# Optimization experiments

Hardware: AMD Instinct MI355X
Metric: run time of the kernel (lower is better)

## Reference

```python
import jax, jax.numpy as jnp
import numpy as np

B, T, C = 4, 2048, 768
H = 12  # n_head; head_dim = C // H = 64


def setup_inputs() -> dict:
    key = jax.random.key(0)
    k1, k2, k3, k4, k5 = jax.random.split(key, 5)
    scale = 0.02
    return {
        "x": jax.random.normal(k1, (B, T, C), dtype=jnp.float32),
        "w_attn": jax.random.normal(k2, (C, 3 * C), dtype=jnp.float32) * scale,
        "b_attn": jax.random.normal(k3, (3 * C,), dtype=jnp.float32) * scale,
        "w_proj": jax.random.normal(k4, (C, C), dtype=jnp.float32) * scale,
        "b_proj": jax.random.normal(k5, (C,), dtype=jnp.float32) * scale,
    }


def reference(x, w_attn, b_attn, w_proj, b_proj):
    Bx, Tx, Cx = x.shape
    hd = Cx // H  # head dim
    qkv = x @ w_attn + b_attn                       # [B, T, 3C]
    q, k, v = jnp.split(qkv, 3, axis=2)
    # [B, T, H, hd] -> [B, H, T, hd]
    q = q.reshape(Bx, Tx, H, hd).transpose(0, 2, 1, 3)
    k = k.reshape(Bx, Tx, H, hd).transpose(0, 2, 1, 3)
    v = v.reshape(Bx, Tx, H, hd).transpose(0, 2, 1, 3)
    att = jnp.einsum('bhqd,bhkd->bhqk', q, k) / jnp.sqrt(jnp.float32(hd))
    causal = jnp.tril(jnp.ones((Tx, Tx), dtype=bool))
    att = jnp.where(causal[None, None, :, :], att, -jnp.inf)
    att = jax.nn.softmax(att, axis=-1)
    y = jnp.einsum('bhqk,bhkd->bhqd', att, v)       # [B, H, T, hd]
    y = y.transpose(0, 2, 1, 3).reshape(Bx, Tx, Cx)
    return y @ w_proj + b_proj
```

## Files before the change

kernel.cpp:

```cpp
#include <hip/hip_runtime.h>
#include <hip/hip_bf16.h>

using f32x4 = __attribute__((ext_vector_type(4))) float;
using s16x8 = __attribute__((ext_vector_type(8))) short;

#define MFMA16x16x32(a, b, c) __builtin_amdgcn_mfma_f32_16x16x32_bf16((a), (b), (c), 0, 0, 0)

#define AS_G(p) ((const __attribute__((address_space(1))) void*)(p))
#define AS_L(p) ((__attribute__((address_space(3))) void*)(p))

#define BARRIER_LGKM() do { \
    asm volatile("s_waitcnt lgkmcnt(0)" ::: "memory"); \
    __builtin_amdgcn_s_barrier(); \
} while (0)

static __device__ __forceinline__ unsigned short f2bf(float f) {
    unsigned int u = __float_as_uint(f);
    u = (u + 0x7fffu + ((u >> 16) & 1u)) >> 16;
    return (unsigned short)u;
}
static __device__ __forceinline__ unsigned int cvt_pk_bf2(float lo, float hi) {
    unsigned int r;
    asm("v_cvt_pk_bf16_f32 %0, %1, %2" : "=v"(r) : "v"(lo), "v"(hi));
    return r;
}
static __device__ __forceinline__ int swz128(int r, int c) { return (r * 128 + c) ^ ((r & 7) << 4); }

__global__ __launch_bounds__(256)
void prologue_kernel(const float* __restrict__ x, unsigned short* __restrict__ xb,
                     const float* __restrict__ w_attn, unsigned short* __restrict__ wTa,
                     const float* __restrict__ w_proj, unsigned short* __restrict__ wTp) {
    __shared__ float tile[32][33];
    const int bid = blockIdx.x, tid = threadIdx.x;
    if (bid < 2048) {
        const int n = 8192 * 768;
        int i = (bid * 256 + tid) * 4;
        const int stride = 2048 * 256 * 4;
        for (; i < n; i += stride) {
            float4 v = *(const float4*)(x + i);
            ushort4 o;
            o.x = f2bf(v.x); o.y = f2bf(v.y); o.z = f2bf(v.z); o.w = f2bf(v.w);
            *(ushort4*)(xb + i) = o;
        }
    } else {
        const float* w; unsigned short* wt; int K, N, bx, by;
        if (bid < 3776) {
            int id = bid - 2048; w = w_attn; wt = wTa; K = 768; N = 2304;
            bx = id % 72; by = id / 72;
        } else {
            int id = bid - 3776; w = w_proj; wt = wTp; K = 768; N = 768;
            bx = id % 24; by = id / 24;
        }
        const int tx = tid & 31, ty = tid >> 5;
        const int n0 = bx * 32, k0 = by * 32;
#pragma unroll
        for (int r = 0; r < 4; r++)
            tile[ty * 4 + r][tx] = w[(size_t)(k0 + ty * 4 + r) * N + n0 + tx];
        __syncthreads();
#pragma unroll
        for (int r = 0; r < 4; r++)
            wt[(size_t)(n0 + ty * 4 + r) * K + k0 + tx] = f2bf(tile[tx][ty * 4 + r]);
    }
}

template <bool OUT_BF16>
__global__ __launch_bounds__(256, 2)
void gemm_bt(const unsigned short* __restrict__ A, const unsigned short* __restrict__ Bt,
             const float* __restrict__ bias, void* __restrict__ Cout,
             unsigned short* __restrict__ Vt,
             int M, int N, int K, int ldc, int qcols, float qscale) {
    __shared__ char smem[65536];
    const int tid = threadIdx.x, wid = tid >> 6, lane = tid & 63;
    const int g = lane >> 4, lr = lane & 15;
    const int m0 = blockIdx.y * 128, n0 = blockIdx.x * 128;
    const int wm = wid >> 1, wn = wid & 1;

    f32x4 acc[4][4];
#pragma unroll
    for (int i = 0; i < 4; i++)
#pragma unroll
        for (int j = 0; j < 4; j++) acc[i][j] = f32x4{0.f, 0.f, 0.f, 0.f};

    const int rbase = lane >> 3;
    const int cSw = ((lane & 7) << 4) ^ (rbase << 4);

    auto STAGE = [&](int buf, int kt) {
        char* base = smem + buf * 32768;
#pragma unroll
        for (int ww = 0; ww < 4; ww++) {
            int w = wid * 4 + ww;
            int r = w * 8 + rbase;
            const unsigned short* srcA = A + (size_t)(m0 + r) * K + kt + (cSw >> 1);
            __builtin_amdgcn_global_load_lds(AS_G(srcA), AS_L(base + w * 1024), 16, 0, 0);
            const unsigned short* srcB = Bt + (size_t)(n0 + r) * K + kt + (cSw >> 1);
            __builtin_amdgcn_global_load_lds(AS_G(srcB), AS_L(base + 16384 + w * 1024), 16, 0, 0);
        }
    };

    const int nk = K >> 6;
    STAGE(0, 0);

    for (int t = 0; t < nk; t++) {
        if (t + 1 < nk) {
            STAGE((t + 1) & 1, (t + 1) << 6);
            asm volatile("s_waitcnt vmcnt(8)" ::: "memory");
        } else {
            asm volatile("s_waitcnt vmcnt(0)" ::: "memory");
        }
        __builtin_amdgcn_s_barrier();
        char* cbase = smem + (t & 1) * 32768;
#pragma unroll
        for (int ks = 0; ks < 2; ks++) {
            s16x8 af[4], bfr[4];
#pragma unroll
            for (int i = 0; i < 4; i++)
                af[i] = *(const s16x8*)(cbase + swz128(wm * 64 + i * 16 + lr, ks * 64 + g * 16));
#pragma unroll
            for (int j = 0; j < 4; j++)
                bfr[j] = *(const s16x8*)(cbase + 16384 + swz128(wn * 64 + j * 16 + lr, ks * 64 + g * 16));
#pragma unroll
            for (int i = 0; i < 4; i++)
#pragma unroll
                for (int j = 0; j < 4; j++)
                    acc[i][j] = MFMA16x16x32(af[i], bfr[j], acc[i][j]);
        }
        BARRIER_LGKM();
    }

#pragma unroll
    for (int j = 0; j < 4; j++) {
        int c = n0 + wn * 64 + j * 16 + lr;
        float bv = bias[c];
        float cscale = (c < qcols) ? qscale : 1.0f;
        if (Vt != nullptr && c >= 1536) {
            int h = (c - 1536) >> 6, d = (c - 1536) & 63;
#pragma unroll
            for (int i = 0; i < 4; i++) {
                int r0 = m0 + wm * 64 + i * 16 + g * 4;
                int bb = r0 >> 11, t0 = r0 & 2047;
                ushort4 o4;
                o4.x = f2bf(acc[i][j][0] + bv);
                o4.y = f2bf(acc[i][j][1] + bv);
                o4.z = f2bf(acc[i][j][2] + bv);
                o4.w = f2bf(acc[i][j][3] + bv);
                *(ushort4*)(Vt + ((((size_t)bb * 12 + h) * 64 + d) << 11) + t0) = o4;
            }
        } else {
#pragma unroll
            for (int i = 0; i < 4; i++) {
#pragma unroll
                for (int rg = 0; rg < 4; rg++) {
                    int r = m0 + wm * 64 + i * 16 + g * 4 + rg;
                    float val = (acc[i][j][rg] + bv) * cscale;
                    if constexpr (OUT_BF16)
                        ((unsigned short*)Cout)[(size_t)r * ldc + c] = f2bf(val);
                    else
                        ((float*)Cout)[(size_t)r * ldc + c] = val;
                }
            }
        }
    }
}

__global__ __launch_bounds__(256, 2)
void attn_kernel(const unsigned short* __restrict__ qk, const unsigned short* __restrict__ Vt,
                 unsigned short* __restrict__ y) {
    __shared__ char smem[49152];
    const int tid = threadIdx.x, wid = tid >> 6, lane = tid & 63;
    const int g = lane >> 4, lr = lane & 15;
    const int T = 2048;

    const int s = blockIdx.x;
    const int xcd = s & 7, i = s >> 3;
    const int grp = xcd * 6 + (i >> 4);
    const int qpi = i & 15;
    const int h = grp % 12, b = grp / 12;
    const int qtA = qpi, qtB = 31 - qpi;
    const int q0A = qtA * 64, q0B = qtB * 64;

    const int krow = tid >> 2;
    const int kcol = (tid & 3) * 32;

    s16x8 vone;
#pragma unroll
    for (int e = 0; e < 8; e++) vone[e] = (short)0x3F80;

    const unsigned short* qrowA = qk + (size_t)(b * T + q0A + wid * 16 + lr) * 1536 + h * 64;
    const unsigned short* qrowB = qk + (size_t)(b * T + q0B + wid * 16 + lr) * 1536 + h * 64;
    s16x8 aqA[2], aqB[2];
    aqA[0] = *(const s16x8*)(qrowA + g * 8);
    aqA[1] = *(const s16x8*)(qrowA + 32 + g * 8);
    aqB[0] = *(const s16x8*)(qrowB + g * 8);
    aqB[1] = *(const s16x8*)(qrowB + 32 + g * 8);

    f32x4 oA[4], oB[4], lsumA, lsumB;
#pragma unroll
    for (int r = 0; r < 4; r++) { oA[r] = f32x4{0.f, 0.f, 0.f, 0.f}; oB[r] = f32x4{0.f, 0.f, 0.f, 0.f}; }
    lsumA = f32x4{0.f, 0.f, 0.f, 0.f};
    lsumB = f32x4{0.f, 0.f, 0.f, 0.f};

    const unsigned short* pkBase = qk + (size_t)(b * T + krow) * 1536 + 768 + h * 64 + (kcol >> 1);
    const unsigned short* pvBase = Vt + ((((size_t)b * 12 + h) * 64 + krow) << 11) + (kcol >> 1);

    const int ntA = qtA + 1, ntB = qtB + 1;

    s16x8 k0 = *(const s16x8*)(pkBase);
    s16x8 k1 = *(const s16x8*)(pkBase + 8);
    s16x8 v0 = *(const s16x8*)(pvBase);
    s16x8 v1 = *(const s16x8*)(pvBase + 8);
    *(s16x8*)(smem + swz128(krow, kcol)) = k0;
    *(s16x8*)(smem + swz128(krow, kcol + 16)) = k1;
    *(s16x8*)(smem + 16384 + swz128(krow, kcol)) = v0;
    *(s16x8*)(smem + 16384 + swz128(krow, kcol + 16)) = v1;
    if (ntB > 1) {
        const unsigned short* pk = pkBase + (size_t)64 * 1536;
        k0 = *(const s16x8*)(pk);
        k1 = *(const s16x8*)(pk + 8);
        const unsigned short* pv = pvBase + 64;
        v0 = *(const s16x8*)(pv);
        v1 = *(const s16x8*)(pv + 8);
    }
    BARRIER_LGKM();

    char* const pbaseB = smem + 32768 + wid * 2048;
    char* const pbaseA = smem + 40960 + wid * 2048;
    const int q_rel = wid * 16 + lr;

    for (int t = 0; t < ntB; t++) {
        char* kbase = smem + (t & 1) * 8192;
        char* vbase = smem + 16384 + (t & 1) * 8192;
        const bool actA = (t < ntA);

        {
            f32x4 st[4];
            __builtin_amdgcn_s_setprio(1);
#pragma unroll
            for (int nf = 0; nf < 4; nf++) {
                f32x4 sf = f32x4{0.f, 0.f, 0.f, 0.f};
#pragma unroll
                for (int ks = 0; ks < 2; ks++) {
                    s16x8 ak = *(const s16x8*)(kbase + swz128(nf * 16 + lr, (ks * 32 + g * 8) * 2));
                    sf = MFMA16x16x32(ak, aqB[ks], sf);
                }
                st[nf] = sf;
            }
            __builtin_amdgcn_s_setprio(0);
            const bool diag = (t == ntB - 1);
#pragma unroll
            for (int nf = 0; nf < 4; nf++)
#pragma unroll
                for (int rg = 0; rg < 4; rg++) {
                    float p = __builtin_amdgcn_exp2f(st[nf][rg]);
                    if (diag && (nf * 16 + g * 4 + rg > q_rel)) p = 0.f;
                    st[nf][rg] = p;
                }
#pragma unroll
            for (int nf = 0; nf < 4; nf++) {
                uint2 dw;
                dw.x = cvt_pk_bf2(st[nf][0], st[nf][1]);
                dw.y = cvt_pk_bf2(st[nf][2], st[nf][3]);
                *(uint2*)(pbaseB + swz128(lr, nf * 32 + g * 8)) = dw;
            }
        }
        if (actA) {
            f32x4 st[4];
            __builtin_amdgcn_s_setprio(1);
#pragma unroll
            for (int nf = 0; nf < 4; nf++) {
                f32x4 sf = f32x4{0.f, 0.f, 0.f, 0.f};
#pragma unroll
                for (int ks = 0; ks < 2; ks++) {
                    s16x8 ak = *(const s16x8*)(kbase + swz128(nf * 16 + lr, (ks * 32 + g * 8) * 2));
                    sf = MFMA16x16x32(ak, aqA[ks], sf);
                }
                st[nf] = sf;
            }
            __builtin_amdgcn_s_setprio(0);
            const bool diag = (t == ntA - 1);
#pragma unroll
            for (int nf = 0; nf < 4; nf++)
#pragma unroll
                for (int rg = 0; rg < 4; rg++) {
                    float p = __builtin_amdgcn_exp2f(st[nf][rg]);
                    if (diag && (nf * 16 + g * 4 + rg > q_rel)) p = 0.f;
                    st[nf][rg] = p;
                }
#pragma unroll
            for (int nf = 0; nf < 4; nf++) {
                uint2 dw;
                dw.x = cvt_pk_bf2(st[nf][0], st[nf][1]);
                dw.y = cvt_pk_bf2(st[nf][2], st[nf][3]);
                *(uint2*)(pbaseA + swz128(lr, nf * 32 + g * 8)) = dw;
            }
        }

        {
            s16x8 pf[2];
#pragma unroll
            for (int ks = 0; ks < 2; ks++)
                pf[ks] = *(const s16x8*)(pbaseB + swz128(lr, ks * 64 + g * 16));
            __builtin_amdgcn_s_setprio(1);
#pragma unroll
            for (int nf = 0; nf < 4; nf++) {
#pragma unroll
                for (int ks = 0; ks < 2; ks++) {
                    s16x8 bv = *(const s16x8*)(vbase + swz128(nf * 16 + lr, ks * 64 + g * 16));
                    oB[nf] = MFMA16x16x32(pf[ks], bv, oB[nf]);
                }
            }
            lsumB = MFMA16x16x32(pf[0], vone, lsumB);
            lsumB = MFMA16x16x32(pf[1], vone, lsumB);
            __builtin_amdgcn_s_setprio(0);
        }
        if (actA) {
            s16x8 pf[2];
#pragma unroll
            for (int ks = 0; ks < 2; ks++)
                pf[ks] = *(const s16x8*)(pbaseA + swz128(lr, ks * 64 + g * 16));
            __builtin_amdgcn_s_setprio(1);
#pragma unroll
            for (int nf = 0; nf < 4; nf++) {
#pragma unroll
                for (int ks = 0; ks < 2; ks++) {
                    s16x8 bv = *(const s16x8*)(vbase + swz128(nf * 16 + lr, ks * 64 + g * 16));
                    oA[nf] = MFMA16x16x32(pf[ks], bv, oA[nf]);
                }
            }
            lsumA = MFMA16x16x32(pf[0], vone, lsumA);
            lsumA = MFMA16x16x32(pf[1], vone, lsumA);
            __builtin_amdgcn_s_setprio(0);
        }

        if (t + 1 < ntB) {
            char* kn = smem + ((t + 1) & 1) * 8192;
            char* vn = smem + 16384 + ((t + 1) & 1) * 8192;
            *(s16x8*)(kn + swz128(krow, kcol)) = k0;
            *(s16x8*)(kn + swz128(krow, kcol + 16)) = k1;
            *(s16x8*)(vn + swz128(krow, kcol)) = v0;
            *(s16x8*)(vn + swz128(krow, kcol + 16)) = v1;
            if (t + 2 < ntB) {
                const unsigned short* pk = pkBase + (size_t)(t + 2) * 64 * 1536;
                k0 = *(const s16x8*)(pk);
                k1 = *(const s16x8*)(pk + 8);
                const unsigned short* pv = pvBase + (t + 2) * 64;
                v0 = *(const s16x8*)(pv);
                v1 = *(const s16x8*)(pv + 8);
            }
        }
        BARRIER_LGKM();
    }

#pragma unroll
    for (int which = 0; which < 2; which++) {
        const f32x4 lsum = which ? lsumB : lsumA;
        const int q0 = which ? q0B : q0A;
        f32x4* o = which ? oB : oA;
        float linv_q[4];
#pragma unroll
        for (int rg = 0; rg < 4; rg++) linv_q[rg] = 1.0f / lsum[rg];
#pragma unroll
        for (int nf = 0; nf < 4; nf++) {
#pragma unroll
            for (int rg = 0; rg < 4; rg++) {
                int row = b * T + q0 + wid * 16 + g * 4 + rg;
                int col = h * 64 + nf * 16 + lr;
                y[(size_t)row * 768 + col] = f2bf(o[nf][rg] * linv_q[rg]);
            }
        }
    }
}

extern "C" void kernel_launch(void* const* d_in, const int* in_sizes, int n_in,
                              void* d_out, int out_size, void* d_ws, size_t ws_size,
                              hipStream_t stream) {
    const float* x      = (const float*)d_in[0];
    const float* w_attn = (const float*)d_in[1];
    const float* b_attn = (const float*)d_in[2];
    const float* w_proj = (const float*)d_in[3];
    const float* b_proj = (const float*)d_in[4];

    char* ws = (char*)d_ws;
    unsigned short* qk  = (unsigned short*)(ws);
    unsigned short* Vt  = (unsigned short*)(ws + 25165824);
    unsigned short* wTa = (unsigned short*)(ws + 37748736);
    unsigned short* wTp = (unsigned short*)(ws + 41287680);

    const bool big = ws_size >= (size_t)55050240;
    unsigned short* xb = (unsigned short*)d_out;
    unsigned short* yb = big ? (unsigned short*)(ws + 42467328)
                             : (unsigned short*)((char*)d_out + 12582912);
    float* projOut = big ? (float*)d_out : (float*)ws;

    prologue_kernel<<<4352, 256, 0, stream>>>(x, xb, w_attn, wTa, w_proj, wTp);

    gemm_bt<true><<<dim3(18, 64), 256, 0, stream>>>(xb, wTa, b_attn, (void*)qk, Vt,
                                                    8192, 2304, 768, 1536, 768, 0.1803368801111244f);
    attn_kernel<<<768, 256, 0, stream>>>(qk, Vt, yb);
    gemm_bt<false><<<dim3(6, 64), 256, 0, stream>>>(yb, wTp, b_proj, (void*)projOut, nullptr,
                                                    8192, 768, 768, 768, 0, 1.0f);
    if (!big)
        hipMemcpyAsync(d_out, projOut, 25165824, hipMemcpyDeviceToDevice, stream);
}
```

Baseline: 123.8 us.

## Remap GEMM blocks per XCD and interleave two query tiles' MFMAs in attention

The GEMM launch becomes a 1D grid. Each block's (m0, n0) is derived from blockIdx so that consecutive blocks landing on the same XCD share an M-row band, which is meant to improve L2 reuse of the A rows on the chiplet. In the attention loop, the QK^T and PV MFMAs for the two query tiles (A and B) are merged into single loops. Each K/V fragment read from LDS is then fed to both tiles, which halves those LDS reads and gives the scheduler independent MFMA chains to interleave. The cost is more live registers, since both score sets are held at once, plus a predicated actA branch inside the inner loops.

Measured after the change: 126.1 us. About the same (+1.8%).

```diff
diff --git a/kernel.cpp b/kernel.cpp
--- a/kernel.cpp
+++ b/kernel.cpp
@@ -72,7 +72,11 @@
     __shared__ char smem[65536];
     const int tid = threadIdx.x, wid = tid >> 6, lane = tid & 63;
     const int g = lane >> 4, lr = lane & 15;
-    const int m0 = blockIdx.y * 128, n0 = blockIdx.x * 128;
+    const int nx = N >> 7;
+    const int ypx = (M >> 7) >> 3;
+    const int xcd = blockIdx.x & 7, ii = blockIdx.x >> 3;
+    const int m0 = (xcd * ypx + ii / nx) * 128;
+    const int n0 = (ii % nx) * 128;
     const int wm = wid >> 1, wn = wid & 1;
 
     f32x4 acc[4][4];
@@ -231,105 +235,86 @@
         char* vbase = smem + 16384 + (t & 1) * 8192;
         const bool actA = (t < ntA);
 
+        f32x4 stB[4], stA[4];
+        __builtin_amdgcn_s_setprio(1);
+#pragma unroll
+        for (int nf = 0; nf < 4; nf++) {
+            f32x4 sB = f32x4{0.f, 0.f, 0.f, 0.f};
+            f32x4 sA = f32x4{0.f, 0.f, 0.f, 0.f};
+#pragma unroll
+            for (int ks = 0; ks < 2; ks++) {
+                s16x8 ak = *(const s16x8*)(kbase + swz128(nf * 16 + lr, (ks * 32 + g * 8) * 2));
+                sB = MFMA16x16x32(ak, aqB[ks], sB);
+                if (actA) sA = MFMA16x16x32(ak, aqA[ks], sA);
+            }
+            stB[nf] = sB;
+            stA[nf] = sA;
+        }
+        __builtin_amdgcn_s_setprio(0);
+
         {
-            f32x4 st[4];
-            __builtin_amdgcn_s_setprio(1);
-#pragma unroll
-            for (int nf = 0; nf < 4; nf++) {
-                f32x4 sf = f32x4{0.f, 0.f, 0.f, 0.f};
-#pragma unroll
-                for (int ks = 0; ks < 2; ks++) {
-                    s16x8 ak = *(const s16x8*)(kbase + swz128(nf * 16 + lr, (ks * 32 + g * 8) * 2));
-                    sf = MFMA16x16x32(ak, aqB[ks], sf);
-                }
-                st[nf] = sf;
-            }
-            __builtin_amdgcn_s_setprio(0);
             const bool diag = (t == ntB - 1);
 #pragma unroll
             for (int nf = 0; nf < 4; nf++)
 #pragma unroll
                 for (int rg = 0; rg < 4; rg++) {
-                    float p = __builtin_amdgcn_exp2f(st[nf][rg]);
+                    float p = __builtin_amdgcn_exp2f(stB[nf][rg]);
                     if (diag && (nf * 16 + g * 4 + rg > q_rel)) p = 0.f;
-                    st[nf][rg] = p;
+                    stB[nf][rg] = p;
                 }
 #pragma unroll
             for (int nf = 0; nf < 4; nf++) {
                 uint2 dw;
-                dw.x = cvt_pk_bf2(st[nf][0], st[nf][1]);
-                dw.y = cvt_pk_bf2(st[nf][2], st[nf][3]);
+                dw.x = cvt_pk_bf2(stB[nf][0], stB[nf][1]);
+                dw.y = cvt_pk_bf2(stB[nf][2], stB[nf][3]);
                 *(uint2*)(pbaseB + swz128(lr, nf * 32 + g * 8)) = dw;
             }
         }
         if (actA) {
-            f32x4 st[4];
-            __builtin_amdgcn_s_setprio(1);
-#pragma unroll
-            for (int nf = 0; nf < 4; nf++) {
-                f32x4 sf = f32x4{0.f, 0.f, 0.f, 0.f};
-#pragma unroll
-                for (int ks = 0; ks < 2; ks++) {
-                    s16x8 ak = *(const s16x8*)(kbase + swz128(nf * 16 + lr, (ks * 32 + g * 8) * 2));
-                    sf = MFMA16x16x32(ak, aqA[ks], sf);
-                }
-                st[nf] = sf;
-            }
-            __builtin_amdgcn_s_setprio(0);
             const bool diag = (t == ntA - 1);
 #pragma unroll
             for (int nf = 0; nf < 4; nf++)
 #pragma unroll
                 for (int rg = 0; rg < 4; rg++) {
-                    float p = __builtin_amdgcn_exp2f(st[nf][rg]);
+                    float p = __builtin_amdgcn_exp2f(stA[nf][rg]);
                     if (diag && (nf * 16 + g * 4 + rg > q_rel)) p = 0.f;
-                    st[nf][rg] = p;
+                    stA[nf][rg] = p;
                 }
 #pragma unroll
             for (int nf = 0; nf < 4; nf++) {
                 uint2 dw;
-                dw.x = cvt_pk_bf2(st[nf][0], st[nf][1]);
-                dw.y = cvt_pk_bf2(st[nf][2], st[nf][3]);
+                dw.x = cvt_pk_bf2(stA[nf][0], stA[nf][1]);
+                dw.y = cvt_pk_bf2(stA[nf][2], stA[nf][3]);
                 *(uint2*)(pbaseA + swz128(lr, nf * 32 + g * 8)) = dw;
             }
         }
 
-        {
-            s16x8 pf[2];
+        s16x8 pfB[2], pfA[2];
+#pragma unroll
+        for (int ks = 0; ks < 2; ks++)
+            pfB[ks] = *(const s16x8*)(pbaseB + swz128(lr, ks * 64 + g * 16));
+        if (actA) {
 #pragma unroll
             for (int ks = 0; ks < 2; ks++)
-                pf[ks] = *(const s16x8*)(pbaseB + swz128(lr, ks * 64 + g * 16));
-            __builtin_amdgcn_s_setprio(1);
-#pragma unroll
-            for (int nf = 0; nf < 4; nf++) {
-#pragma unroll
-                for (int ks = 0; ks < 2; ks++) {
-                    s16x8 bv = *(const s16x8*)(vbase + swz128(nf * 16 + lr, ks * 64 + g * 16));
-                    oB[nf] = MFMA16x16x32(pf[ks], bv, oB[nf]);
-                }
-            }
-            lsumB = MFMA16x16x32(pf[0], vone, lsumB);
-            lsumB = MFMA16x16x32(pf[1], vone, lsumB);
-            __builtin_amdgcn_s_setprio(0);
-        }
+                pfA[ks] = *(const s16x8*)(pbaseA + swz128(lr, ks * 64 + g * 16));
+        }
+        __builtin_amdgcn_s_setprio(1);
+#pragma unroll
+        for (int nf = 0; nf < 4; nf++) {
+#pragma unroll
+            for (int ks = 0; ks < 2; ks++) {
+                s16x8 bv = *(const s16x8*)(vbase + swz128(nf * 16 + lr, ks * 64 + g * 16));
+                oB[nf] = MFMA16x16x32(pfB[ks], bv, oB[nf]);
+                if (actA) oA[nf] = MFMA16x16x32(pfA[ks], bv, oA[nf]);
+            }
+        }
+        lsumB = MFMA16x16x32(pfB[0], vone, lsumB);
+        lsumB = MFMA16x16x32(pfB[1], vone, lsumB);
         if (actA) {
-            s16x8 pf[2];
-#pragma unroll
-            for (int ks = 0; ks < 2; ks++)
-                pf[ks] = *(const s16x8*)(pbaseA + swz128(lr, ks * 64 + g * 16));
-            __builtin_amdgcn_s_setprio(1);
-#pragma unroll
-            for (int nf = 0; nf < 4; nf++) {
-#pragma unroll
-                for (int ks = 0; ks < 2; ks++) {
-                    s16x8 bv = *(const s16x8*)(vbase + swz128(nf * 16 + lr, ks * 64 + g * 16));
-                    oA[nf] = MFMA16x16x32(pf[ks], bv, oA[nf]);
-                }
-            }
-            lsumA = MFMA16x16x32(pf[0], vone, lsumA);
-            lsumA = MFMA16x16x32(pf[1], vone, lsumA);
-            __builtin_amdgcn_s_setprio(0);
-        }
+            lsumA = MFMA16x16x32(pfA[0], vone, lsumA);
+            lsumA = MFMA16x16x32(pfA[1], vone, lsumA);
+        }
+        __builtin_amdgcn_s_setprio(0);
 
         if (t + 1 < ntB) {
             char* kn = smem + ((t + 1) & 1) * 8192;
@@ -393,11 +378,11 @@
 
     prologue_kernel<<<4352, 256, 0, stream>>>(x, xb, w_attn, wTa, w_proj, wTp);
 
-    gemm_bt<true><<<dim3(18, 64), 256, 0, stream>>>(xb, wTa, b_attn, (void*)qk, Vt,
-                                                    8192, 2304, 768, 1536, 768, 0.1803368801111244f);
+    gemm_bt<true><<<1152, 256, 0, stream>>>(xb, wTa, b_attn, (void*)qk, Vt,
+                                            8192, 2304, 768, 1536, 768, 0.1803368801111244f);
     attn_kernel<<<768, 256, 0, stream>>>(qk, Vt, yb);
-    gemm_bt<false><<<dim3(6, 64), 256, 0, stream>>>(yb, wTp, b_proj, (void*)projOut, nullptr,
-                                                    8192, 768, 768, 768, 0, 1.0f);
+    gemm_bt<false><<<384, 256, 0, stream>>>(yb, wTp, b_proj, (void*)projOut, nullptr,
+                                            8192, 768, 768, 768, 0, 1.0f);
     if (!big)
         hipMemcpyAsync(d_out, projOut, 25165824, hipMemcpyDeviceToDevice, stream);
 }
```

## Halve GEMM K-tile to raise occupancy and remap blocks per XCD

Applied to the files above, without the earlier changes.

The GEMM K-step drops from 64 to 32, which halves shared memory to 32KB so that four blocks per CU can be resident (launch bounds raised to 4). Loading is restructured so each thread issues four global_load_lds ops covering both the A and B tiles. The grid becomes 1D, and block IDs are remapped so that each XCD handles a contiguous band of M rows for better L2 reuse. In exchange there are twice as many barrier and sync iterations per tile, and register pressure may rise under the tighter launch bound.

After: 122.7 us. About the same (-0.9%).

```diff
diff --git a/kernel.cpp b/kernel.cpp
--- a/kernel.cpp
+++ b/kernel.cpp
@@ -64,15 +64,19 @@
 }
 
 template <bool OUT_BF16>
-__global__ __launch_bounds__(256, 2)
+__global__ __launch_bounds__(256, 4)
 void gemm_bt(const unsigned short* __restrict__ A, const unsigned short* __restrict__ Bt,
              const float* __restrict__ bias, void* __restrict__ Cout,
              unsigned short* __restrict__ Vt,
              int M, int N, int K, int ldc, int qcols, float qscale) {
-    __shared__ char smem[65536];
+    __shared__ char smem[32768];
     const int tid = threadIdx.x, wid = tid >> 6, lane = tid & 63;
     const int g = lane >> 4, lr = lane & 15;
-    const int m0 = blockIdx.y * 128, n0 = blockIdx.x * 128;
+    const int nx = N >> 7;
+    const int ypx = (M >> 7) >> 3;
+    const int xcd = blockIdx.x & 7, ii = blockIdx.x >> 3;
+    const int m0 = (xcd * ypx + ii / nx) * 128;
+    const int n0 = (ii % nx) * 128;
     const int wm = wid >> 1, wn = wid & 1;
 
     f32x4 acc[4][4];
@@ -81,49 +85,45 @@
 #pragma unroll
         for (int j = 0; j < 4; j++) acc[i][j] = f32x4{0.f, 0.f, 0.f, 0.f};
 
-    const int rbase = lane >> 3;
-    const int cSw = ((lane & 7) << 4) ^ (rbase << 4);
+    const int rr = tid >> 3;
+    const int cS = ((tid & 7) << 4) ^ ((rr & 7) << 4);
+    const bool isB = cS >= 64;
+    const int colE = (isB ? cS - 64 : cS) >> 1;
+    const unsigned short* bp = isB ? (Bt + (size_t)(n0 + rr) * K + colE)
+                                   : (A + (size_t)(m0 + rr) * K + colE);
 
     auto STAGE = [&](int buf, int kt) {
-        char* base = smem + buf * 32768;
-#pragma unroll
-        for (int ww = 0; ww < 4; ww++) {
-            int w = wid * 4 + ww;
-            int r = w * 8 + rbase;
-            const unsigned short* srcA = A + (size_t)(m0 + r) * K + kt + (cSw >> 1);
-            __builtin_amdgcn_global_load_lds(AS_G(srcA), AS_L(base + w * 1024), 16, 0, 0);
-            const unsigned short* srcB = Bt + (size_t)(n0 + r) * K + kt + (cSw >> 1);
-            __builtin_amdgcn_global_load_lds(AS_G(srcB), AS_L(base + 16384 + w * 1024), 16, 0, 0);
-        }
+        char* base = smem + buf * 16384 + wid * 1024;
+#pragma unroll
+        for (int i = 0; i < 4; i++)
+            __builtin_amdgcn_global_load_lds(AS_G(bp + (size_t)i * 32 * K + kt),
+                                             AS_L(base + i * 4096), 16, 0, 0);
     };
 
-    const int nk = K >> 6;
+    const int nk = K >> 5;
     STAGE(0, 0);
 
     for (int t = 0; t < nk; t++) {
         if (t + 1 < nk) {
-            STAGE((t + 1) & 1, (t + 1) << 6);
-            asm volatile("s_waitcnt vmcnt(8)" ::: "memory");
+            STAGE((t + 1) & 1, (t + 1) << 5);
+            asm volatile("s_waitcnt vmcnt(4)" ::: "memory");
         } else {
             asm volatile("s_waitcnt vmcnt(0)" ::: "memory");
         }
         __builtin_amdgcn_s_barrier();
-        char* cbase = smem + (t & 1) * 32768;
-#pragma unroll
-        for (int ks = 0; ks < 2; ks++) {
-            s16x8 af[4], bfr[4];
-#pragma unroll
-            for (int i = 0; i < 4; i++)
-                af[i] = *(const s16x8*)(cbase + swz128(wm * 64 + i * 16 + lr, ks * 64 + g * 16));
+        char* cbase = smem + (t & 1) * 16384;
+        s16x8 af[4], bfr[4];
+#pragma unroll
+        for (int i = 0; i < 4; i++)
+            af[i] = *(const s16x8*)(cbase + swz128(wm * 64 + i * 16 + lr, g * 16));
+#pragma unroll
+        for (int j = 0; j < 4; j++)
+            bfr[j] = *(const s16x8*)(cbase + swz128(wn * 64 + j * 16 + lr, 64 + g * 16));
+#pragma unroll
+        for (int i = 0; i < 4; i++)
 #pragma unroll
             for (int j = 0; j < 4; j++)
-                bfr[j] = *(const s16x8*)(cbase + 16384 + swz128(wn * 64 + j * 16 + lr, ks * 64 + g * 16));
-#pragma unroll
-            for (int i = 0; i < 4; i++)
-#pragma unroll
-                for (int j = 0; j < 4; j++)
-                    acc[i][j] = MFMA16x16x32(af[i], bfr[j], acc[i][j]);
-        }
+                acc[i][j] = MFMA16x16x32(af[i], bfr[j], acc[i][j]);
         BARRIER_LGKM();
     }
 
@@ -393,11 +393,11 @@
 
     prologue_kernel<<<4352, 256, 0, stream>>>(x, xb, w_attn, wTa, w_proj, wTp);
 
-    gemm_bt<true><<<dim3(18, 64), 256, 0, stream>>>(xb, wTa, b_attn, (void*)qk, Vt,
-                                                    8192, 2304, 768, 1536, 768, 0.1803368801111244f);
+    gemm_bt<true><<<1152, 256, 0, stream>>>(xb, wTa, b_attn, (void*)qk, Vt,
+                                            8192, 2304, 768, 1536, 768, 0.1803368801111244f);
     attn_kernel<<<768, 256, 0, stream>>>(qk, Vt, yb);
-    gemm_bt<false><<<dim3(6, 64), 256, 0, stream>>>(yb, wTp, b_proj, (void*)projOut, nullptr,
-                                                    8192, 768, 768, 768, 0, 1.0f);
+    gemm_bt<false><<<384, 256, 0, stream>>>(yb, wTp, b_proj, (void*)projOut, nullptr,
+                                            8192, 768, 768, 768, 0, 1.0f);
     if (!big)
         hipMemcpyAsync(d_out, projOut, 25165824, hipMemcpyDeviceToDevice, stream);
 }
```

## Remap GEMM tiles per XCD and stage V-transpose output through LDS

Applied to the files above, without the earlier changes.

Blocks are launched on a 1D grid and remapped so that each XCD (blockIdx mod 8) handles a contiguous band of M rows, improving L2 locality of A tiles within an XCD. The V-transpose epilogue of the QKV GEMM now writes the tile into swizzled shared memory first, then emits 16-byte contiguous stores along the time axis instead of scattered 8-byte stores. This adds a barrier and LDS traffic in the epilogue and assumes M is divisible by 1024 and that the grid size matches the remap.

Measured after the change: 117.9 us. -4.8%, faster.

```diff
diff --git a/kernel.cpp b/kernel.cpp
--- a/kernel.cpp
+++ b/kernel.cpp
@@ -25,6 +25,7 @@
     return r;
 }
 static __device__ __forceinline__ int swz128(int r, int c) { return (r * 128 + c) ^ ((r & 7) << 4); }
+static __device__ __forceinline__ int swz256v(int r, int c) { return (r * 256 + c) ^ ((r & 7) << 4); }
 
 __global__ __launch_bounds__(256)
 void prologue_kernel(const float* __restrict__ x, unsigned short* __restrict__ xb,
@@ -72,7 +73,11 @@
     __shared__ char smem[65536];
     const int tid = threadIdx.x, wid = tid >> 6, lane = tid & 63;
     const int g = lane >> 4, lr = lane & 15;
-    const int m0 = blockIdx.y * 128, n0 = blockIdx.x * 128;
+    const int nx = N >> 7;
+    const int ypx = (M >> 7) >> 3;
+    const int xcd = blockIdx.x & 7, ii = blockIdx.x >> 3;
+    const int m0 = (xcd * ypx + ii / nx) * 128;
+    const int n0 = (ii % nx) * 128;
     const int wm = wid >> 1, wn = wid & 1;
 
     f32x4 acc[4][4];
@@ -127,25 +132,38 @@
         BARRIER_LGKM();
     }
 
-#pragma unroll
-    for (int j = 0; j < 4; j++) {
-        int c = n0 + wn * 64 + j * 16 + lr;
-        float bv = bias[c];
-        float cscale = (c < qcols) ? qscale : 1.0f;
-        if (Vt != nullptr && c >= 1536) {
-            int h = (c - 1536) >> 6, d = (c - 1536) & 63;
+    if (Vt != nullptr && n0 >= 1536) {
+#pragma unroll
+        for (int j = 0; j < 4; j++) {
+            int dl = wn * 64 + j * 16 + lr;
+            float bv = bias[n0 + dl];
 #pragma unroll
             for (int i = 0; i < 4; i++) {
-                int r0 = m0 + wm * 64 + i * 16 + g * 4;
-                int bb = r0 >> 11, t0 = r0 & 2047;
+                int tl = wm * 64 + i * 16 + g * 4;
                 ushort4 o4;
                 o4.x = f2bf(acc[i][j][0] + bv);
                 o4.y = f2bf(acc[i][j][1] + bv);
                 o4.z = f2bf(acc[i][j][2] + bv);
                 o4.w = f2bf(acc[i][j][3] + bv);
-                *(ushort4*)(Vt + ((((size_t)bb * 12 + h) * 64 + d) << 11) + t0) = o4;
-            }
-        } else {
+                *(ushort4*)(smem + swz256v(dl, tl * 2)) = o4;
+            }
+        }
+        __syncthreads();
+        const int bb = m0 >> 11, t0 = m0 & 2047;
+#pragma unroll
+        for (int it = 0; it < 8; it++) {
+            int dl = it * 16 + wid * 4 + g;
+            int dg = (n0 - 1536) + dl;
+            int hh = dg >> 6, dd = dg & 63;
+            s16x8 v = *(const s16x8*)(smem + swz256v(dl, lr * 16));
+            *(s16x8*)(Vt + ((((size_t)bb * 12 + hh) * 64 + dd) << 11) + t0 + lr * 8) = v;
+        }
+    } else {
+#pragma unroll
+        for (int j = 0; j < 4; j++) {
+            int c = n0 + wn * 64 + j * 16 + lr;
+            float bv = bias[c];
+            float cscale = (c < qcols) ? qscale : 1.0f;
 #pragma unroll
             for (int i = 0; i < 4; i++) {
 #pragma unroll
@@ -393,11 +411,11 @@
 
     prologue_kernel<<<4352, 256, 0, stream>>>(x, xb, w_attn, wTa, w_proj, wTp);
 
-    gemm_bt<true><<<dim3(18, 64), 256, 0, stream>>>(xb, wTa, b_attn, (void*)qk, Vt,
-                                                    8192, 2304, 768, 1536, 768, 0.1803368801111244f);
+    gemm_bt<true><<<1152, 256, 0, stream>>>(xb, wTa, b_attn, (void*)qk, Vt,
+                                            8192, 2304, 768, 1536, 768, 0.1803368801111244f);
     attn_kernel<<<768, 256, 0, stream>>>(qk, Vt, yb);
-    gemm_bt<false><<<dim3(6, 64), 256, 0, stream>>>(yb, wTp, b_proj, (void*)projOut, nullptr,
-                                                    8192, 768, 768, 768, 0, 1.0f);
+    gemm_bt<false><<<384, 256, 0, stream>>>(yb, wTp, b_proj, (void*)projOut, nullptr,
+                                            8192, 768, 768, 768, 0, 1.0f);
     if (!big)
         hipMemcpyAsync(d_out, projOut, 25165824, hipMemcpyDeviceToDevice, stream);
 }
```
